# Performance work log

Measured on AMD Instinct MI355X. Metric: run time of the kernel, lower is better.

## Reference

```python
import jax, jax.numpy as jnp
import numpy as np

# Circuit hyperparameters (match init_kwargs)
N_QUBITS = 10
N_LAYERS = 5          # hardware_efficient_ansatz layers (data re-uploading)
N_ACTIONS = 2         # CartPole-v1 discrete action space
BETA = 1.0
DIM = 2 ** N_QUBITS

# Bit table: wire 0 is the most-significant bit (PennyLane convention).
_bits = ((np.arange(DIM)[:, None] >> (N_QUBITS - 1 - np.arange(N_QUBITS))) & 1)

# Diagonal of the ring of CZ gates: product over pairs (i, i+1 mod n) of (-1)^{b_i b_j}.
_s = np.ones(DIM)
for _i in range(N_QUBITS):
    _j = (_i + 1) % N_QUBITS
    _s *= 1.0 - 2.0 * (_bits[:, _i] * _bits[:, _j])
CZ_DIAG = jnp.asarray(_s, dtype=jnp.complex64)

# Z^{\otimes n} observable diagonal: (-1)^{popcount(k)}
Z_SIGN = jnp.asarray(1.0 - 2.0 * (_bits.sum(1) % 2), dtype=jnp.float32)


def _rx(t):
    c = jnp.cos(0.5 * t).astype(jnp.complex64)
    s = jnp.sin(0.5 * t).astype(jnp.complex64)
    return jnp.stack([jnp.stack([c, -1j * s], -1), jnp.stack([-1j * s, c], -1)], -2)


def _ry(t):
    c = jnp.cos(0.5 * t).astype(jnp.complex64)
    s = jnp.sin(0.5 * t).astype(jnp.complex64)
    return jnp.stack([jnp.stack([c, -s], -1), jnp.stack([s, c], -1)], -2)


def _rz(t):
    e = jnp.exp(-0.5j * t.astype(jnp.complex64))
    z = jnp.zeros_like(e)
    return jnp.stack([jnp.stack([e, z], -1), jnp.stack([z, jnp.conj(e)], -1)], -2)


def _apply_1q(state, U, q):
    """Apply a single-qubit gate on wire q. state: [B, 2^n]; U: [2,2] or [B,2,2]."""
    B = state.shape[0]
    s = state.reshape(B, 2 ** q, 2, -1)
    if U.ndim == 2:
        s = jnp.einsum('ij,bljr->blir', U, s)
    else:
        s = jnp.einsum('bij,bljr->blir', U, s)
    return s.reshape(B, DIM)


def _variational_layer(state, t):
    """Per-qubit Rx,Ry,Rz rotations (t: [n_qubits,3]) followed by a CZ ring."""
    for q in range(N_QUBITS):
        U = _rz(t[q, 2]) @ _ry(t[q, 1]) @ _rx(t[q, 0])  # RX applied first
        state = _apply_1q(state, U, q)
    return state * CZ_DIAG


def setup_inputs() -> dict:
    key = jax.random.key(0)
    k1, k2 = jax.random.split(key)
    x = jax.random.normal(k1, (2048, N_QUBITS), jnp.float32)
    # _theta = rand(total_theta) * pi ; total_theta = (L+1)*n*3
    theta = jax.random.uniform(k2, ((N_LAYERS + 1) * N_QUBITS * 3,), jnp.float32) * np.pi
    # _lambda = ones(total_inputs) ; total_inputs = L*n
    lam = jnp.ones((N_LAYERS * N_QUBITS,), jnp.float32)
    # Alternating(n_actions): weight row initialized to alternating signs
    w = jnp.asarray([[(-1.0) ** i for i in range(N_ACTIONS)]], jnp.float32)
    return {"x": x, "theta": theta, "lam": lam, "w": w}


def reference(x, theta, lam, w):
    B = x.shape[0]
    th = theta.reshape(N_LAYERS + 1, N_QUBITS, 3)
    lm = lam.reshape(N_LAYERS, N_QUBITS)  # scaled_inputs = x_tiled * lambda
    state = jnp.zeros((B, DIM), jnp.complex64).at[:, 0].set(1.0)
    for l in range(N_LAYERS):
        state = _variational_layer(state, th[l])
        ang = x * lm[l]                      # [B, n] encoding angles for this layer
        for q in range(N_QUBITS):
            state = _apply_1q(state, _rx(ang[:, q]), q)
    state = _variational_layer(state, th[N_LAYERS])
    # <Z x Z x ... x Z>
    exp_z = jnp.sum((state.real ** 2 + state.imag ** 2) * Z_SIGN, axis=1)  # [B]
    logits = exp_z[:, None] * w * BETA       # [B,1] @ [1,n_actions], scaled by beta
    return jax.nn.softmax(logits, axis=1)
```

## Files before the change

### kernel.cpp

```cpp
#include <hip/hip_runtime.h>

#define NQ 10
#define NL 5

typedef float v2f __attribute__((ext_vector_type(2)));

__device__ __forceinline__ v2f sp(float s) { v2f r = { s, s }; return r; }

template <int M>
__device__ __forceinline__ float lane_xor_direct(float v) {
    unsigned u = __float_as_uint(v);
    if constexpr (M == 1) {
        return __uint_as_float((unsigned)__builtin_amdgcn_update_dpp(0, (int)u, 0xB1, 0xF, 0xF, true));
    } else if constexpr (M == 2) {
        return __uint_as_float((unsigned)__builtin_amdgcn_update_dpp(0, (int)u, 0x4E, 0xF, 0xF, true));
    } else if constexpr (M == 4) {
        return __uint_as_float((unsigned)__builtin_amdgcn_ds_swizzle((int)u, 0x101F));
    } else {
        return __uint_as_float((unsigned)__builtin_amdgcn_update_dpp(0, (int)u, 0x128, 0xF, 0xF, true));
    }
}

template <int M>
__device__ __forceinline__ void lane_swap_pair(float v, float& r0, float& r1) {
    unsigned u = __float_as_uint(v);
    if constexpr (M == 16) {
        auto r = __builtin_amdgcn_permlane16_swap(u, u, false, false);
        r0 = __uint_as_float(r[0]); r1 = __uint_as_float(r[1]);
    } else {
        auto r = __builtin_amdgcn_permlane32_swap(u, u, false, false);
        r0 = __uint_as_float(r[0]); r1 = __uint_as_float(r[1]);
    }
}

template <int M>
__device__ __forceinline__ float lane_xor(float v, int lane) {
    if constexpr (M < 16) {
        return lane_xor_direct<M>(v);
    } else {
        float r0, r1;
        lane_swap_pair<M>(v, r0, r1);
        return (lane & M) ? r0 : r1;
    }
}

__device__ __forceinline__ void make_u(float tx, float ty, float tz,
                                       float& u00r, float& u00i, float& u01r, float& u01i,
                                       float& u10r, float& u10i, float& u11r, float& u11i) {
    float cx, sx, cy, sy, cz, sz;
    __sincosf(0.5f * tx, &sx, &cx);
    __sincosf(0.5f * ty, &sy, &cy);
    __sincosf(0.5f * tz, &sz, &cz);
    u00r =  cz * cy * cx + sz * sy * sx;
    u00i =  cz * sy * sx - sz * cy * cx;
    u01r = -cz * sy * cx - sz * cy * sx;
    u01i =  sz * sy * cx - cz * cy * sx;
    u10r = -u01r;  u10i =  u01i;
    u11r =  u00r;  u11i = -u00i;
}

__global__ void pqc_setup(const float* __restrict__ theta, float* __restrict__ gm) {
    int g = threadIdx.x;
    if (g >= (NL + 1) * NQ) return;
    const float* th = theta + g * 3;
    float u00r, u00i, u01r, u01i, u10r, u10i, u11r, u11i;
    make_u(th[0], th[1], th[2], u00r, u00i, u01r, u01i, u10r, u10i, u11r, u11i);
    float* o = gm + g * 16;
    o[0] = u00r;  o[1] = u00i;  o[2] = u01r;  o[3] = u01i;
    o[4] = u10r;  o[5] = u10i;  o[6] = u11r;  o[7] = u11i;
    o[8]  = u01i; o[9]  = -u01r; o[10] = u00i; o[11] = -u00r;
    o[12] = u11i; o[13] = -u11r; o[14] = u10i; o[15] = -u10r;
}

template <int P>
__device__ __forceinline__ void apply_p(v2f fr[8], v2f fi[8], const float wv[8], int lane) {
    const float w00r = wv[0], w00i = wv[1], w01r = wv[2], w01i = wv[3];
    const float w10r = wv[4], w10i = wv[5], w11r = wv[6], w11i = wv[7];
    if constexpr (P == 0) {
        v2f c0r = { w00r, w11r }, c0i = { w00i, w11i };
        v2f c1r = { w01r, w10r }, c1i = { w01i, w10i };
#pragma unroll
        for (int j = 0; j < 8; ++j) {
            v2f ar = fr[j], ai = fi[j];
            v2f srp = ar.yx, sip = ai.yx;
            fr[j] = c0r * ar - c0i * ai + c1r * srp - c1i * sip;
            fi[j] = c0r * ai + c0i * ar + c1r * sip + c1i * srp;
        }
    } else if constexpr (P < 4) {
        constexpr int LJ = 1 << (P - 1);
        v2f a00r = sp(w00r), a00i = sp(w00i), a01r = sp(w01r), a01i = sp(w01i);
        v2f a10r = sp(w10r), a10i = sp(w10i), a11r = sp(w11r), a11i = sp(w11i);
#pragma unroll
        for (int base = 0; base < 8; ++base) {
            if (base & LJ) continue;
            v2f a0r = fr[base], a0i = fi[base];
            v2f a1r = fr[base | LJ], a1i = fi[base | LJ];
            fr[base]      = a00r * a0r - a00i * a0i + a01r * a1r - a01i * a1i;
            fi[base]      = a00r * a0i + a00i * a0r + a01r * a1i + a01i * a1r;
            fr[base | LJ] = a10r * a0r - a10i * a0i + a11r * a1r - a11i * a1i;
            fi[base | LJ] = a10r * a0i + a10i * a0r + a11r * a1i + a11i * a1r;
        }
    } else if constexpr (P < 8) {
        constexpr int M = 1 << (P - 4);
        const int bit = (lane >> (P - 4)) & 1;
        v2f pr = sp(bit ? w11r : w00r), pi = sp(bit ? w11i : w00i);
        v2f qr = sp(bit ? w10r : w01r), qi = sp(bit ? w10i : w01i);
#pragma unroll
        for (int j = 0; j < 8; ++j) {
            v2f ofr, ofi;
            ofr.x = lane_xor_direct<M>(fr[j].x);
            ofr.y = lane_xor_direct<M>(fr[j].y);
            ofi.x = lane_xor_direct<M>(fi[j].x);
            ofi.y = lane_xor_direct<M>(fi[j].y);
            v2f nr = pr * fr[j] - pi * fi[j] + qr * ofr - qi * ofi;
            v2f ni = pr * fi[j] + pi * fr[j] + qr * ofi + qi * ofr;
            fr[j] = nr;
            fi[j] = ni;
        }
    } else {
        constexpr int M = 1 << (P - 4);
        const bool hi = (lane & M) != 0;
        v2f cAr = sp(hi ? w10r : w00r), cAi = sp(hi ? w10i : w00i);
        v2f cBr = sp(hi ? w11r : w01r), cBi = sp(hi ? w11i : w01i);
#pragma unroll
        for (int j = 0; j < 8; ++j) {
            float a0x, a1x, a0y, a1y, b0x, b1x, b0y, b1y;
            lane_swap_pair<M>(fr[j].x, a0x, a1x);
            lane_swap_pair<M>(fr[j].y, a0y, a1y);
            lane_swap_pair<M>(fi[j].x, b0x, b1x);
            lane_swap_pair<M>(fi[j].y, b0y, b1y);
            v2f A0r = { a0x, a0y }, A1r = { a1x, a1y };
            v2f A0i = { b0x, b0y }, A1i = { b1x, b1y };
            fr[j] = cAr * A0r - cAi * A0i + cBr * A1r - cBi * A1i;
            fi[j] = cAr * A0i + cAi * A0r + cBr * A1i + cBi * A1r;
        }
    }
}

#define GATE2(qq, PP)                                                              \
    {                                                                              \
        const float* g = gl + (qq) * 16;                                           \
        float W0[8], W1[8];                                                        \
        _Pragma("unroll")                                                          \
        for (int t = 0; t < 8; ++t) {                                              \
            W0[t] = cc0[qq] * g[t] + ss0[qq] * g[8 + t];                           \
            W1[t] = cc1[qq] * g[t] + ss1[qq] * g[8 + t];                           \
        }                                                                          \
        apply_p<PP>(fr0, fi0, W0, lane);                                           \
        apply_p<PP>(fr1, fi1, W1, lane);                                           \
    }

__global__ void __launch_bounds__(64, 2) pqc_kernel(const float* __restrict__ x,
                                                    const float* __restrict__ lam,
                                                    const float* __restrict__ w,
                                                    const float* __restrict__ gm,
                                                    float* __restrict__ out, int B) {
    const int lane = threadIdx.x;
    const int b0 = blockIdx.x * 2;
    const int b1 = b0 + 1;

    v2f fr0[8], fi0[8], fr1[8], fi1[8];
#pragma unroll
    for (int j = 0; j < 8; ++j) {
        fr0[j] = sp(0.f); fi0[j] = sp(0.f);
        fr1[j] = sp(0.f); fi1[j] = sp(0.f);
    }
    if (lane == 0) { fr0[0].x = 1.f; fr1[0].x = 1.f; }

    v2f sv[8];
    unsigned zmask = 0;
#pragma unroll
    for (int j = 0; j < 8; ++j) {
#pragma unroll
        for (int h = 0; h < 2; ++h) {
            int k = (lane << 4) | (2 * j + h);
            int par = (__popc(k & (k >> 1)) + ((k & (k >> 9)) & 1)) & 1;
            float s = __uint_as_float(0x3f800000u | ((unsigned)par << 31));
            if (h == 0) sv[j].x = s; else sv[j].y = s;
            zmask |= (unsigned)(__popc(k) & 1) << (2 * j + h);
        }
    }

    float xr0[NQ], xr1[NQ];
#pragma unroll
    for (int q = 0; q < NQ; ++q) {
        xr0[q] = x[b0 * NQ + q];
        xr1[q] = x[b1 * NQ + q];
    }

    for (int l = 0; l <= NL; ++l) {
        const float* gl = gm + l * NQ * 16;
        const float* lm = lam + (l > 0 ? (l - 1) * NQ : 0);
        const float en = (l > 0) ? 0.5f : 0.0f;
        float cc0[NQ], ss0[NQ], cc1[NQ], ss1[NQ];
#pragma unroll
        for (int q = 0; q < NQ; ++q) {
            __sincosf(en * xr0[q] * lm[q], &ss0[q], &cc0[q]);
            __sincosf(en * xr1[q] * lm[q], &ss1[q], &cc1[q]);
        }
        GATE2(0, 9) GATE2(1, 8) GATE2(2, 7) GATE2(3, 6) GATE2(4, 5)
        GATE2(5, 4) GATE2(6, 3) GATE2(7, 2) GATE2(8, 1) GATE2(9, 0)
#pragma unroll
        for (int j = 0; j < 8; ++j) {
            fr0[j] *= sv[j]; fi0[j] *= sv[j];
            fr1[j] *= sv[j]; fi1[j] *= sv[j];
        }
    }

    v2f acc0 = sp(0.f), acc1 = sp(0.f);
#pragma unroll
    for (int j = 0; j < 8; ++j) {
        v2f zs;
        zs.x = __uint_as_float(0x3f800000u | (((zmask >> (2 * j)) & 1u) << 31));
        zs.y = __uint_as_float(0x3f800000u | (((zmask >> (2 * j + 1)) & 1u) << 31));
        acc0 += zs * (fr0[j] * fr0[j] + fi0[j] * fi0[j]);
        acc1 += zs * (fr1[j] * fr1[j] + fi1[j] * fi1[j]);
    }
    float ez0 = acc0.x + acc0.y;
    float ez1 = acc1.x + acc1.y;
    ez0 += lane_xor<1>(ez0, lane);   ez1 += lane_xor<1>(ez1, lane);
    ez0 += lane_xor<2>(ez0, lane);   ez1 += lane_xor<2>(ez1, lane);
    ez0 += lane_xor<4>(ez0, lane);   ez1 += lane_xor<4>(ez1, lane);
    ez0 += lane_xor<8>(ez0, lane);   ez1 += lane_xor<8>(ez1, lane);
    ez0 += lane_xor<16>(ez0, lane);  ez1 += lane_xor<16>(ez1, lane);
    ez0 += lane_xor<32>(ez0, lane);  ez1 += lane_xor<32>(ez1, lane);

    if (lane == 0) {
        float w0 = w[0], w1 = w[1];
        {
            float l0 = ez0 * w0, l1 = ez0 * w1;
            float m = fmaxf(l0, l1);
            float e0 = __expf(l0 - m), e1 = __expf(l1 - m);
            float inv = 1.f / (e0 + e1);
            out[2 * b0 + 0] = e0 * inv;
            out[2 * b0 + 1] = e1 * inv;
        }
        {
            float l0 = ez1 * w0, l1 = ez1 * w1;
            float m = fmaxf(l0, l1);
            float e0 = __expf(l0 - m), e1 = __expf(l1 - m);
            float inv = 1.f / (e0 + e1);
            out[2 * b1 + 0] = e0 * inv;
            out[2 * b1 + 1] = e1 * inv;
        }
    }
}

extern "C" void kernel_launch(void* const* d_in, const int* in_sizes, int n_in,
                              void* d_out, int out_size, void* d_ws, size_t ws_size,
                              hipStream_t stream) {
    const float* x     = (const float*)d_in[0];
    const float* theta = (const float*)d_in[1];
    const float* lam   = (const float*)d_in[2];
    const float* w     = (const float*)d_in[3];
    float* out = (float*)d_out;
    float* gm  = (float*)d_ws;

    const int B = in_sizes[0] / NQ;
    hipLaunchKernelGGL(pqc_setup, dim3(1), dim3(64), 0, stream, theta, gm);
    hipLaunchKernelGGL(pqc_kernel, dim3(B / 2), dim3(64), 0, stream,
                       x, lam, w, gm, out, B);
}
```

Before: 101.2 us.

## Process one sample per wavefront instead of two and vectorize gate coefficient build

Each 64-lane block now simulates a single batch element instead of two, launching B blocks rather than B/2. This halves the register-resident state per wave, which should raise occupancy and parallelism at the cost of losing the interleaved ILP between two independent states. The gate weight mixing now uses v2f loads, the layer loop is explicitly not unrolled, and the xor-4 lane exchange uses two masked DPP row ops instead of ds_swizzle.

```diff
diff --git a/kernel.cpp b/kernel.cpp
--- a/kernel.cpp
+++ b/kernel.cpp
@@ -15,7 +15,9 @@
     } else if constexpr (M == 2) {
         return __uint_as_float((unsigned)__builtin_amdgcn_update_dpp(0, (int)u, 0x4E, 0xF, 0xF, true));
     } else if constexpr (M == 4) {
-        return __uint_as_float((unsigned)__builtin_amdgcn_ds_swizzle((int)u, 0x101F));
+        int t = __builtin_amdgcn_update_dpp(0, (int)u, 0x104, 0xF, 0x5, false);
+        t     = __builtin_amdgcn_update_dpp(t, (int)u, 0x114, 0xF, 0xA, false);
+        return __uint_as_float((unsigned)t);
     } else {
         return __uint_as_float((unsigned)__builtin_amdgcn_update_dpp(0, (int)u, 0x128, 0xF, 0xF, true));
     }
@@ -137,17 +139,16 @@
     }
 }
 
-#define GATE2(qq, PP)                                                              \
+#define GATE(qq, PP)                                                               \
     {                                                                              \
         const float* g = gl + (qq) * 16;                                           \
-        float W0[8], W1[8];                                                        \
-        _Pragma("unroll")                                                          \
-        for (int t = 0; t < 8; ++t) {                                              \
-            W0[t] = cc0[qq] * g[t] + ss0[qq] * g[8 + t];                           \
-            W1[t] = cc1[qq] * g[t] + ss1[qq] * g[8 + t];                           \
-        }                                                                          \
-        apply_p<PP>(fr0, fi0, W0, lane);                                           \
-        apply_p<PP>(fr1, fi1, W1, lane);                                           \
+        v2f c = sp(cc[qq]), s = sp(ss[qq]);                                        \
+        v2f w0 = c * *(const v2f*)(g + 0) + s * *(const v2f*)(g + 8);              \
+        v2f w1 = c * *(const v2f*)(g + 2) + s * *(const v2f*)(g + 10);             \
+        v2f w2 = c * *(const v2f*)(g + 4) + s * *(const v2f*)(g + 12);             \
+        v2f w3 = c * *(const v2f*)(g + 6) + s * *(const v2f*)(g + 14);             \
+        const float W[8] = { w0.x, w0.y, w1.x, w1.y, w2.x, w2.y, w3.x, w3.y };     \
+        apply_p<PP>(fr, fi, W, lane);                                              \
     }
 
 __global__ void __launch_bounds__(64, 2) pqc_kernel(const float* __restrict__ x,
@@ -156,16 +157,12 @@
                                                     const float* __restrict__ gm,
                                                     float* __restrict__ out, int B) {
     const int lane = threadIdx.x;
-    const int b0 = blockIdx.x * 2;
-    const int b1 = b0 + 1;
-
-    v2f fr0[8], fi0[8], fr1[8], fi1[8];
-#pragma unroll
-    for (int j = 0; j < 8; ++j) {
-        fr0[j] = sp(0.f); fi0[j] = sp(0.f);
-        fr1[j] = sp(0.f); fi1[j] = sp(0.f);
-    }
-    if (lane == 0) { fr0[0].x = 1.f; fr1[0].x = 1.f; }
+    const int b = blockIdx.x;
+
+    v2f fr[8], fi[8];
+#pragma unroll
+    for (int j = 0; j < 8; ++j) { fr[j] = sp(0.f); fi[j] = sp(0.f); }
+    if (lane == 0) fr[0].x = 1.f;
 
     v2f sv[8];
     unsigned zmask = 0;
@@ -181,68 +178,48 @@
         }
     }
 
-    float xr0[NQ], xr1[NQ];
-#pragma unroll
-    for (int q = 0; q < NQ; ++q) {
-        xr0[q] = x[b0 * NQ + q];
-        xr1[q] = x[b1 * NQ + q];
-    }
-
+    float xr[NQ];
+#pragma unroll
+    for (int q = 0; q < NQ; ++q) xr[q] = x[b * NQ + q];
+
+#pragma clang loop unroll(disable)
     for (int l = 0; l <= NL; ++l) {
         const float* gl = gm + l * NQ * 16;
         const float* lm = lam + (l > 0 ? (l - 1) * NQ : 0);
         const float en = (l > 0) ? 0.5f : 0.0f;
-        float cc0[NQ], ss0[NQ], cc1[NQ], ss1[NQ];
-#pragma unroll
-        for (int q = 0; q < NQ; ++q) {
-            __sincosf(en * xr0[q] * lm[q], &ss0[q], &cc0[q]);
-            __sincosf(en * xr1[q] * lm[q], &ss1[q], &cc1[q]);
-        }
-        GATE2(0, 9) GATE2(1, 8) GATE2(2, 7) GATE2(3, 6) GATE2(4, 5)
-        GATE2(5, 4) GATE2(6, 3) GATE2(7, 2) GATE2(8, 1) GATE2(9, 0)
-#pragma unroll
-        for (int j = 0; j < 8; ++j) {
-            fr0[j] *= sv[j]; fi0[j] *= sv[j];
-            fr1[j] *= sv[j]; fi1[j] *= sv[j];
-        }
-    }
-
-    v2f acc0 = sp(0.f), acc1 = sp(0.f);
+        float cc[NQ], ss[NQ];
+#pragma unroll
+        for (int q = 0; q < NQ; ++q)
+            __sincosf(en * xr[q] * lm[q], &ss[q], &cc[q]);
+        GATE(0, 9) GATE(1, 8) GATE(2, 7) GATE(3, 6) GATE(4, 5)
+        GATE(5, 4) GATE(6, 3) GATE(7, 2) GATE(8, 1) GATE(9, 0)
+#pragma unroll
+        for (int j = 0; j < 8; ++j) { fr[j] *= sv[j]; fi[j] *= sv[j]; }
+    }
+
+    v2f acc = sp(0.f);
 #pragma unroll
     for (int j = 0; j < 8; ++j) {
         v2f zs;
         zs.x = __uint_as_float(0x3f800000u | (((zmask >> (2 * j)) & 1u) << 31));
         zs.y = __uint_as_float(0x3f800000u | (((zmask >> (2 * j + 1)) & 1u) << 31));
-        acc0 += zs * (fr0[j] * fr0[j] + fi0[j] * fi0[j]);
-        acc1 += zs * (fr1[j] * fr1[j] + fi1[j] * fi1[j]);
-    }
-    float ez0 = acc0.x + acc0.y;
-    float ez1 = acc1.x + acc1.y;
-    ez0 += lane_xor<1>(ez0, lane);   ez1 += lane_xor<1>(ez1, lane);
-    ez0 += lane_xor<2>(ez0, lane);   ez1 += lane_xor<2>(ez1, lane);
-    ez0 += lane_xor<4>(ez0, lane);   ez1 += lane_xor<4>(ez1, lane);
-    ez0 += lane_xor<8>(ez0, lane);   ez1 += lane_xor<8>(ez1, lane);
-    ez0 += lane_xor<16>(ez0, lane);  ez1 += lane_xor<16>(ez1, lane);
-    ez0 += lane_xor<32>(ez0, lane);  ez1 += lane_xor<32>(ez1, lane);
+        acc += zs * (fr[j] * fr[j] + fi[j] * fi[j]);
+    }
+    float ez = acc.x + acc.y;
+    ez += lane_xor<1>(ez, lane);
+    ez += lane_xor<2>(ez, lane);
+    ez += lane_xor<4>(ez, lane);
+    ez += lane_xor<8>(ez, lane);
+    ez += lane_xor<16>(ez, lane);
+    ez += lane_xor<32>(ez, lane);
 
     if (lane == 0) {
-        float w0 = w[0], w1 = w[1];
-        {
-            float l0 = ez0 * w0, l1 = ez0 * w1;
-            float m = fmaxf(l0, l1);
-            float e0 = __expf(l0 - m), e1 = __expf(l1 - m);
-            float inv = 1.f / (e0 + e1);
-            out[2 * b0 + 0] = e0 * inv;
-            out[2 * b0 + 1] = e1 * inv;
-        }
-        {
-            float l0 = ez1 * w0, l1 = ez1 * w1;
-            float m = fmaxf(l0, l1);
-            float e0 = __expf(l0 - m), e1 = __expf(l1 - m);
-            float inv = 1.f / (e0 + e1);
-            out[2 * b1 + 0] = e0 * inv;
-            out[2 * b1 + 1] = e1 * inv;
-        }
+        float l0 = ez * w[0], l1 = ez * w[1];
+        float m = fmaxf(l0, l1);
+        float e0 = __expf(l0 - m), e1 = __expf(l1 - m);
+        float inv = 1.f / (e0 + e1);
+        out[2 * b + 0] = e0 * inv;
+        out[2 * b + 1] = e1 * inv;
     }
 }
 
@@ -258,6 +235,6 @@
 
     const int B = in_sizes[0] / NQ;
     hipLaunchKernelGGL(pqc_setup, dim3(1), dim3(64), 0, stream, theta, gm);
-    hipLaunchKernelGGL(pqc_kernel, dim3(B / 2), dim3(64), 0, stream,
+    hipLaunchKernelGGL(pqc_kernel, dim3(B), dim3(64), 0, stream,
                        x, lam, w, gm, out, B);
 }
```

Result: faster. 90.14 us (-10.9%).
